# Performance work log

Measured on AMD Instinct MI355X. Metric: run time of the kernel, lower is better.

The kernel has to match this reference:

```python
import jax, jax.numpy as jnp
import numpy as np

# All unordered pairs of 6 ligand sites (octahedral complex)
PAIRS = np.array([(i, j) for i in range(6) for j in range(i + 1, 6)], dtype=np.int32)  # [15, 2]

B, N_LIGS, D = 32768, 6, 64
IN_DIM = D + 2 * D  # core + lig_i + lig_j = 192
H1, H2 = 64, 32


def setup_inputs() -> dict:
    key = jax.random.key(0)
    ks = jax.random.split(key, 8)
    s = 0.05  # small init scale for numerical sanity
    return {
        "core": jax.random.normal(ks[0], (B, D), dtype=jnp.float32),
        "ligs": jax.random.normal(ks[1], (B, N_LIGS, D), dtype=jnp.float32),
        "W1": jax.random.normal(ks[2], (IN_DIM, H1), dtype=jnp.float32) * s,
        "b1": jnp.zeros((H1,), dtype=jnp.float32),
        "W2": jax.random.normal(ks[3], (H1, H2), dtype=jnp.float32) * s,
        "b2": jnp.zeros((H2,), dtype=jnp.float32),
        "W3": jax.random.normal(ks[4], (H2, 1), dtype=jnp.float32) * s,
        "b3": jnp.zeros((1,), dtype=jnp.float32),
    }


def _mlp(x, W1, b1, W2, b2, W3, b3):
    # Dense(softplus) -> Dense(softplus) -> Dense(1, linear); dropout is identity at inference
    h = jax.nn.softplus(x @ W1 + b1)
    h = jax.nn.softplus(h @ W2 + b2)
    return h @ W3 + b3  # [..., 1]


def reference(core, ligs, W1, b1, W2, b2, W3, b3):
    i_idx = jnp.asarray(PAIRS[:, 0])
    j_idx = jnp.asarray(PAIRS[:, 1])
    P = PAIRS.shape[0]
    li = ligs[:, i_idx, :]  # [B, P, D]
    lj = ligs[:, j_idx, :]  # [B, P, D]
    c = jnp.broadcast_to(core[:, None, :], (core.shape[0], P, core.shape[1]))
    x1 = jnp.concatenate([c, li, lj], axis=-1)  # [B, P, 3D]
    x2 = jnp.concatenate([c, lj, li], axis=-1)  # [B, P, 3D]
    res = 0.5 * (_mlp(x1, W1, b1, W2, b2, W3, b3) + _mlp(x2, W1, b1, W2, b2, W3, b3))  # [B, P, 1]
    return jnp.sum(res, axis=1)  # [B, 1]
```

## Files before the change

### kernel.cpp

```cpp
#include <hip/hip_runtime.h>
#include <hip/hip_fp16.h>
#include <stdint.h>


typedef __attribute__((ext_vector_type(8))) _Float16 f16x8;
typedef __attribute__((ext_vector_type(2))) __fp16   fp16v2;
typedef __attribute__((ext_vector_type(4))) float    f32x4;
typedef __attribute__((ext_vector_type(4))) unsigned int u32x4;

constexpr int   BPB       = 32;
constexpr int   NT        = 1024;
constexpr int   T_STRIDE  = 1680;
constexpr int   Y_OFF     = BPB * T_STRIDE;
constexpr int   LDS_BYTES = Y_OFF + 128;

constexpr int   WS_W1T   = 0;
constexpr int   WS_W2T   = 24576;
constexpr int   WS_B1    = 28672;
constexpr int   WS_B2    = 28928;
constexpr int   WS_W3    = 29056;
constexpr int   WS_BYTES = 29184;

constexpr float L2E = 1.4426950408889634f;
constexpr float LN2 = 0.6931471805599453f;

constexpr unsigned long long I_BITS =
  (0ull<<0)|(0ull<<3)|(0ull<<6)|(0ull<<9)|(0ull<<12)|
  (1ull<<15)|(1ull<<18)|(1ull<<21)|(1ull<<24)|
  (2ull<<27)|(2ull<<30)|(2ull<<33)|
  (3ull<<36)|(3ull<<39)|(4ull<<42);
constexpr unsigned long long J_BITS =
  (1ull<<0)|(2ull<<3)|(3ull<<6)|(4ull<<9)|(5ull<<12)|
  (2ull<<15)|(3ull<<18)|(4ull<<21)|(5ull<<24)|
  (3ull<<27)|(4ull<<30)|(5ull<<33)|
  (4ull<<36)|(5ull<<39)|(5ull<<42);

__device__ __forceinline__ float sp2(float s) {
  float t = __builtin_amdgcn_exp2f(s);
  return __builtin_amdgcn_logf(1.0f + t);
}

__device__ __forceinline__ __half2 h1pair(__half2 u, __half2 a, __half2 b,
                                          __half2 one2) {
  __half2 s = __hadd2(__hadd2(u, a), b);
  __half2 t = h2exp2(s);
  return h2log2(__hadd2(one2, t));
}

__global__ __launch_bounds__(256)
void prep(const float* __restrict__ W1, const float* __restrict__ b1,
          const float* __restrict__ W2, const float* __restrict__ b2,
          const float* __restrict__ W3, char* __restrict__ ws)
{
  const int t = (int)(blockIdx.x * blockDim.x + threadIdx.x);
  uint16_t* w1t = (uint16_t*)(ws + WS_W1T);
  uint16_t* w2t = (uint16_t*)(ws + WS_W2T);
  float*    b1s = (float*)(ws + WS_B1);
  float*    b2s = (float*)(ws + WS_B2);
  float*    w3s = (float*)(ws + WS_W3);
  if (t < 12288) {
    const int d = t >> 6, n = t & 63;
    const int slab = d >> 6;
    w1t[(slab * 64 + n) * 64 + (d & 63)] =
        __half_as_ushort(__float2half(W1[t] * L2E));
  } else if (t < 14336) {
    const int e = t - 12288;
    const int k = e >> 5, m = e & 31;
    w2t[m * 64 + k] = __half_as_ushort(__float2half(W2[e]));
  } else if (t < 14400) {
    b1s[t - 14336] = b1[t - 14336] * L2E;
  } else if (t < 14432) {
    b2s[t - 14400] = b2[t - 14400] * L2E;
  } else if (t < 14464) {
    w3s[t - 14432] = W3[t - 14432] * LN2;
  }
}

__global__ __launch_bounds__(NT, 8)
void tb_fused(const float* __restrict__ core, const float* __restrict__ ligs,
              const float* __restrict__ b3,   const char* __restrict__ ws,
              float* __restrict__ out)
{
  extern __shared__ char smem[];
  const int tid  = (int)threadIdx.x;
  const int lane = tid & 63;
  const int ln   = lane & 15;
  const int qd   = lane >> 4;
  const int wv   = __builtin_amdgcn_readfirstlane(tid >> 6);
  const int b0   = (int)blockIdx.x * BPB;

  const uint16_t* w1t = (const uint16_t*)(ws + WS_W1T);
  const uint16_t* w2t = (const uint16_t*)(ws + WS_W2T);
  const float*    b1s = (const float*)(ws + WS_B1);
  const float*    b2s = (const float*)(ws + WS_B2);
  const float*    w3s = (const float*)(ws + WS_W3);

  float* yred = (float*)(smem + Y_OFF);
  if (tid < BPB) yred[tid] = 0.0f;

  #pragma unroll 1
  for (int jj = 0; jj < 2; ++jj) {
    const int j = wv + 16 * jj;
    if (j >= 26) break;
    int xr, sl, mt, trow;
    if (j < 2)  { xr = 0; sl = 0; mt = j; trow = 0; }
    else        { const int e = j - 2; xr = (e >> 2) + 1; sl = 1 + ((e >> 1) & 1);
                  mt = e & 1; trow = (sl == 1) ? xr : 6 + xr; }

    const float* src = (xr == 0)
        ? (core + (size_t)(b0 + mt * 16 + ln) * 64)
        : (ligs + ((size_t)(b0 + mt * 16 + ln) * 6 + (size_t)(xr - 1)) * 64);

    union AF { f16x8 v; fp16v2 p[4]; } Afr[2];
    #pragma unroll
    for (int ks = 0; ks < 2; ++ks) {
      const float4 f0 = *(const float4*)(src + ks * 32 + qd * 8);
      const float4 f1 = *(const float4*)(src + ks * 32 + qd * 8 + 4);
      Afr[ks].p[0] = __builtin_amdgcn_cvt_pkrtz(f0.x, f0.y);
      Afr[ks].p[1] = __builtin_amdgcn_cvt_pkrtz(f0.z, f0.w);
      Afr[ks].p[2] = __builtin_amdgcn_cvt_pkrtz(f1.x, f1.y);
      Afr[ks].p[3] = __builtin_amdgcn_cvt_pkrtz(f1.z, f1.w);
    }

    #pragma unroll
    for (int nt = 0; nt < 4; ++nt) {
      f32x4 c = {0.f, 0.f, 0.f, 0.f};
      #pragma unroll
      for (int ks = 0; ks < 2; ++ks) {
        const f16x8 Bf = *(const f16x8*)(w1t +
            (sl * 64 + nt * 16 + ln) * 64 + ks * 32 + qd * 8);
        c = __builtin_amdgcn_mfma_f32_16x16x32_f16(Afr[ks].v, Bf, c, 0, 0, 0);
      }
      const float bias = (trow == 0) ? b1s[nt * 16 + ln] : 0.0f;
      #pragma unroll
      for (int reg = 0; reg < 4; ++reg) {
        const int b = mt * 16 + qd * 4 + reg;
        *(uint16_t*)(smem + (size_t)b * T_STRIDE + trow * 128 + (nt * 16 + ln) * 2) =
            __half_as_ushort(__float2half(c[reg] + bias));
      }
    }
  }

  f16x8 W2f[2][2];
  #pragma unroll
  for (int nt = 0; nt < 2; ++nt)
    #pragma unroll
    for (int ks = 0; ks < 2; ++ks)
      W2f[nt][ks] = *(const f16x8*)(w2t + (nt * 16 + ln) * 64 + ks * 32 + qd * 8);
  float b2v[2], w3v[2];
  #pragma unroll
  for (int nt = 0; nt < 2; ++nt) {
    b2v[nt] = b2s[nt * 16 + ln];
    w3v[nt] = w3s[nt * 16 + ln];
  }

  __syncthreads();

  const int mtw = wv & 1;
  const int qr  = wv >> 1;
  const __half2 one2 = __float2half2_rn(1.0f);
  const char* Tb  = smem + (size_t)(mtw * 16 + ln) * T_STRIDE;
  const int koff  = qd * 16;

  float yacc[4] = {0.f, 0.f, 0.f, 0.f};

  #pragma unroll 2
  for (int t3 = 0; t3 < 4; ++t3) {
    const int q = qr + 8 * t3;
    if (q >= 30) break;
    const int p  = q >> 1;
    const int iv = (int)((I_BITS >> (3 * p)) & 7ull);
    const int jv = (int)((J_BITS >> (3 * p)) & 7ull);
    const int An = (q & 1) ? jv : iv;
    const int Bn = (q & 1) ? iv : jv;
    const char* TA = Tb + (1 + An) * 128;
    const char* TB = Tb + (7 + Bn) * 128;

    union U4 { u32x4 u; __half2 h[4]; };
    U4 du0, da0, db0, du1, da1, db1;
    du0.u = *(const u32x4*)(Tb + koff);
    da0.u = *(const u32x4*)(TA + koff);
    db0.u = *(const u32x4*)(TB + koff);
    du1.u = *(const u32x4*)(Tb + 64 + koff);
    da1.u = *(const u32x4*)(TA + 64 + koff);
    db1.u = *(const u32x4*)(TB + 64 + koff);

    union { f16x8 v; __half2 h[4]; } A0, A1;
    #pragma unroll
    for (int w = 0; w < 4; ++w) A0.h[w] = h1pair(du0.h[w], da0.h[w], db0.h[w], one2);
    #pragma unroll
    for (int w = 0; w < 4; ++w) A1.h[w] = h1pair(du1.h[w], da1.h[w], db1.h[w], one2);

    f32x4 c0 = {0.f, 0.f, 0.f, 0.f};
    f32x4 c1 = {0.f, 0.f, 0.f, 0.f};
    c0 = __builtin_amdgcn_mfma_f32_16x16x32_f16(A0.v, W2f[0][0], c0, 0, 0, 0);
    c0 = __builtin_amdgcn_mfma_f32_16x16x32_f16(A1.v, W2f[0][1], c0, 0, 0, 0);
    c1 = __builtin_amdgcn_mfma_f32_16x16x32_f16(A0.v, W2f[1][0], c1, 0, 0, 0);
    c1 = __builtin_amdgcn_mfma_f32_16x16x32_f16(A1.v, W2f[1][1], c1, 0, 0, 0);

    #pragma unroll
    for (int reg = 0; reg < 4; ++reg) {
      yacc[reg] += sp2(c0[reg] + b2v[0]) * w3v[0]
                 + sp2(c1[reg] + b2v[1]) * w3v[1];
    }
  }

  #pragma unroll
  for (int reg = 0; reg < 4; ++reg) {
    float v = yacc[reg];
    v += __shfl_xor(v, 1);
    v += __shfl_xor(v, 2);
    v += __shfl_xor(v, 4);
    v += __shfl_xor(v, 8);
    yacc[reg] = v;
  }
  if (ln == 0) {
    #pragma unroll
    for (int reg = 0; reg < 4; ++reg)
      atomicAdd(&yred[mtw * 16 + qd * 4 + reg], yacc[reg]);
  }
  __syncthreads();
  if (tid < BPB) out[b0 + tid] = 0.5f * yred[tid] + 15.0f * b3[0];
}

extern "C" void kernel_launch(void* const* d_in, const int* in_sizes, int n_in,
                              void* d_out, int out_size, void* d_ws, size_t ws_size,
                              hipStream_t stream) {
  const float* core = (const float*)d_in[0];
  const float* ligs = (const float*)d_in[1];
  const float* W1   = (const float*)d_in[2];
  const float* b1   = (const float*)d_in[3];
  const float* W2   = (const float*)d_in[4];
  const float* b2   = (const float*)d_in[5];
  const float* W3   = (const float*)d_in[6];
  const float* b3   = (const float*)d_in[7];
  float* out = (float*)d_out;
  char*  ws  = (char*)d_ws;

  const int B = in_sizes[0] / 64;
  const int grid = B / BPB;

  prep<<<dim3(57), dim3(256), 0, stream>>>(W1, b1, W2, b2, W3, ws);

  (void)hipFuncSetAttribute((const void*)tb_fused,
                            hipFuncAttributeMaxDynamicSharedMemorySize, LDS_BYTES);
  tb_fused<<<dim3(grid), dim3(NT), LDS_BYTES, stream>>>(
      core, ligs, b3, ws, out);
}
```

Measured before the change: 146.5 us.

## Stage W1 in padded LDS and load each input row once for both slabs

```diff
diff --git a/kernel.cpp b/kernel.cpp
--- a/kernel.cpp
+++ b/kernel.cpp
@@ -11,7 +11,9 @@
 constexpr int   BPB       = 32;
 constexpr int   NT        = 1024;
 constexpr int   T_STRIDE  = 1680;
-constexpr int   Y_OFF     = BPB * T_STRIDE;
+constexpr int   WT_RS     = 72;
+constexpr int   WT_OFF    = BPB * T_STRIDE;
+constexpr int   Y_OFF     = WT_OFF + 192 * WT_RS * 2;
 constexpr int   LDS_BYTES = Y_OFF + 128;
 
 constexpr int   WS_W1T   = 0;
@@ -89,24 +91,26 @@
   const int wv   = __builtin_amdgcn_readfirstlane(tid >> 6);
   const int b0   = (int)blockIdx.x * BPB;
 
-  const uint16_t* w1t = (const uint16_t*)(ws + WS_W1T);
   const uint16_t* w2t = (const uint16_t*)(ws + WS_W2T);
   const float*    b1s = (const float*)(ws + WS_B1);
   const float*    b2s = (const float*)(ws + WS_B2);
   const float*    w3s = (const float*)(ws + WS_W3);
 
   float* yred = (float*)(smem + Y_OFF);
+
+  #pragma unroll
+  for (int rep = 0; rep < 3; ++rep) {
+    const int c   = tid + rep * NT;
+    const int row = c >> 4, col = c & 15;
+    *(uint2*)(smem + WT_OFF + row * (WT_RS * 2) + col * 8) =
+        *(const uint2*)(ws + WS_W1T + row * 128 + col * 8);
+  }
   if (tid < BPB) yred[tid] = 0.0f;
-
-  #pragma unroll 1
-  for (int jj = 0; jj < 2; ++jj) {
-    const int j = wv + 16 * jj;
-    if (j >= 26) break;
-    int xr, sl, mt, trow;
-    if (j < 2)  { xr = 0; sl = 0; mt = j; trow = 0; }
-    else        { const int e = j - 2; xr = (e >> 2) + 1; sl = 1 + ((e >> 1) & 1);
-                  mt = e & 1; trow = (sl == 1) ? xr : 6 + xr; }
-
+  __syncthreads();
+
+  if (wv < 14) {
+    const int xr = wv >> 1;
+    const int mt = wv & 1;
     const float* src = (xr == 0)
         ? (core + (size_t)(b0 + mt * 16 + ln) * 64)
         : (ligs + ((size_t)(b0 + mt * 16 + ln) * 6 + (size_t)(xr - 1)) * 64);
@@ -122,21 +126,27 @@
       Afr[ks].p[3] = __builtin_amdgcn_cvt_pkrtz(f1.z, f1.w);
     }
 
-    #pragma unroll
-    for (int nt = 0; nt < 4; ++nt) {
-      f32x4 c = {0.f, 0.f, 0.f, 0.f};
+    const int sl_lo = (xr == 0) ? 0 : 1;
+    const int sl_hi = (xr == 0) ? 0 : 2;
+    #pragma unroll 1
+    for (int sl = sl_lo; sl <= sl_hi; ++sl) {
+      const int trow = (xr == 0) ? 0 : ((sl == 1) ? xr : 6 + xr);
       #pragma unroll
-      for (int ks = 0; ks < 2; ++ks) {
-        const f16x8 Bf = *(const f16x8*)(w1t +
-            (sl * 64 + nt * 16 + ln) * 64 + ks * 32 + qd * 8);
-        c = __builtin_amdgcn_mfma_f32_16x16x32_f16(Afr[ks].v, Bf, c, 0, 0, 0);
-      }
-      const float bias = (trow == 0) ? b1s[nt * 16 + ln] : 0.0f;
-      #pragma unroll
-      for (int reg = 0; reg < 4; ++reg) {
-        const int b = mt * 16 + qd * 4 + reg;
-        *(uint16_t*)(smem + (size_t)b * T_STRIDE + trow * 128 + (nt * 16 + ln) * 2) =
-            __half_as_ushort(__float2half(c[reg] + bias));
+      for (int nt = 0; nt < 4; ++nt) {
+        f32x4 c = {0.f, 0.f, 0.f, 0.f};
+        #pragma unroll
+        for (int ks = 0; ks < 2; ++ks) {
+          const f16x8 Bf = *(const f16x8*)(smem + WT_OFF +
+              ((sl * 64 + nt * 16 + ln) * WT_RS + ks * 32 + qd * 8) * 2);
+          c = __builtin_amdgcn_mfma_f32_16x16x32_f16(Afr[ks].v, Bf, c, 0, 0, 0);
+        }
+        const float bias = (trow == 0) ? b1s[nt * 16 + ln] : 0.0f;
+        #pragma unroll
+        for (int reg = 0; reg < 4; ++reg) {
+          const int b = mt * 16 + qd * 4 + reg;
+          *(uint16_t*)(smem + (size_t)b * T_STRIDE + trow * 128 + (nt * 16 + ln) * 2) =
+              __half_as_ushort(__float2half(c[reg] + bias));
+        }
       }
     }
   }
```

Result: faster. 124.9 us (-14.7%).
